# Performance work log

Measured on AMD Instinct MI355X. Metric: run time of the kernel, lower is better.

Reference implementation:

```python
import jax, jax.numpy as jnp
import numpy as np

ROPE_BASE = 10000.0

def _rope(x, positions):
    # x: (B, h, T, d); standard half-split rotary embedding with d_key = d
    d = x.shape[-1]
    inv_freq = 1.0 / (ROPE_BASE ** (jnp.arange(0, d // 2, dtype=jnp.float32) / (d // 2)))
    ang = positions.astype(jnp.float32)[:, None] * inv_freq[None, :]  # (T, d/2)
    cos, sin = jnp.cos(ang), jnp.sin(ang)
    x1, x2 = x[..., : d // 2], x[..., d // 2 :]
    return jnp.concatenate([x1 * cos - x2 * sin, x1 * sin + x2 * cos], axis=-1)


def setup_inputs() -> dict:
    key = jax.random.key(0)
    k1, k2, k3 = jax.random.split(key, 3)
    B, T, d, h = 2, 2048, 768, 8
    std = d ** -0.5
    x = jax.random.normal(k1, (B, T, d), dtype=jnp.float32)
    M = jax.random.normal(k2, (d, h * d), dtype=jnp.float32) * std
    V = jax.random.normal(k3, (d, h * d), dtype=jnp.float32) * std
    positions = jnp.arange(T, dtype=jnp.int32)
    return {"x": x, "M": M, "V": V, "positions": positions}


def reference(x, M, V, positions):
    B, T, d = x.shape
    h = M.shape[1] // d
    scale = 1.0 / jnp.sqrt(jnp.float32(d))
    # Q = RoPE(X @ M), K = RoPE(X) broadcast across heads, val = X @ V
    Q = (x @ M).reshape(B, T, h, d).transpose(0, 2, 1, 3)   # (B,h,T,d)
    val = (x @ V).reshape(B, T, h, d).transpose(0, 2, 1, 3)  # (B,h,T,d)
    K = jnp.broadcast_to(x[:, None, :, :], (B, h, T, d))     # (B,h,T,d)
    Q = _rope(Q, positions)
    K = _rope(K, positions)
    scores = jnp.einsum("bhqd,bhkd->bhqk", Q, K) * scale     # (B,h,T,T)
    causal = jnp.tril(jnp.ones((T, T), dtype=bool))          # True = keep
    scores = jnp.where(causal[None, None], scores, -jnp.inf)
    attn = jax.nn.softmax(scores, axis=-1)
    out = jnp.einsum("bhqk,bhkd->bhqd", attn, val)
    return out.sum(axis=1)  # sum over heads -> (B,T,d)
```

## Files before the change

### kernel.cpp

```cpp
#include <hip/hip_runtime.h>
#include <hip/hip_bf16.h>

typedef __bf16 bf16x8 __attribute__((ext_vector_type(8)));
typedef float f32x4 __attribute__((ext_vector_type(4)));
typedef float f32x16 __attribute__((ext_vector_type(16)));

#define SCALE 0.03608439182435161f
#define NEGINF (-1e30f)

static __device__ __forceinline__ ushort f2bf(float f) {
    union { float f; unsigned u; } v; v.f = f;
    unsigned r = (v.u + 0x7fff + ((v.u >> 16) & 1)) >> 16;
    return (ushort)r;
}
static __device__ __forceinline__ float bf2f(ushort u) {
    union { unsigned u; float f; } v; v.u = ((unsigned)u) << 16;
    return v.f;
}

static __device__ __forceinline__ void gload16(const void* g, void* lds) {
    __builtin_amdgcn_global_load_lds((const __attribute__((address_space(1))) void*)g,
                                     (__attribute__((address_space(3))) void*)lds, 16, 0, 0);
}

#define PHASEB do { asm volatile("s_waitcnt vmcnt(0) lgkmcnt(0)" ::: "memory"); \
                    __builtin_amdgcn_s_barrier(); \
                    asm volatile("" ::: "memory"); } while (0)
#define BARL do { asm volatile("s_waitcnt lgkmcnt(0)" ::: "memory"); \
                  __builtin_amdgcn_s_barrier(); \
                  asm volatile("" ::: "memory"); } while (0)

__global__ void k_convx(const float* __restrict__ x, ushort* __restrict__ xb, int n4) {
    int i = blockIdx.x * blockDim.x + threadIdx.x;
    if (i >= n4) return;
    float4 v = ((const float4*)x)[i];
    ushort4 o; o.x = f2bf(v.x); o.y = f2bf(v.y); o.z = f2bf(v.z); o.w = f2bf(v.w);
    ((ushort4*)xb)[i] = o;
}

__global__ void k_tconv(const float* __restrict__ in, ushort* __restrict__ out, int R, int C) {
    __shared__ float ts[32][33];
    int r0 = blockIdx.x * 32, c0 = blockIdx.y * 32;
    int lr = threadIdx.x >> 5, lc = threadIdx.x & 31;
#pragma unroll
    for (int i = 0; i < 4; i++) ts[lr + i * 8][lc] = in[(r0 + lr + i * 8) * C + c0 + lc];
    __syncthreads();
#pragma unroll
    for (int i = 0; i < 4; i++) out[(c0 + lr + i * 8) * R + r0 + lc] = f2bf(ts[lc][lr + i * 8]);
}

template <int EPI>
__global__ __launch_bounds__(256) void k_gemm(const ushort* __restrict__ A,
                                              const ushort* __restrict__ Bt,
                                              ushort* __restrict__ out) {
    __shared__ ushort As[128 * 32];
    __shared__ ushort Bs[128 * 32];
    const int m0 = blockIdx.x * 128, n0 = blockIdx.y * 128;
    const int tid = threadIdx.x, lane = tid & 63, wid = tid >> 6;
    const int wm = (wid >> 1) * 64, wn = (wid & 1) * 64;
    const int l15 = lane & 15, l4 = lane >> 4;
    const int srow = tid >> 2, scol = (tid & 3) * 8;
    f32x4 acc[4][4] = {};

    for (int kt = 0; kt < 768; kt += 32) {
        gload16(&A[(size_t)(m0 + srow) * 768 + kt + scol],       (char*)As + wid * 1024);
        gload16(&A[(size_t)(m0 + 64 + srow) * 768 + kt + scol],  (char*)As + 4096 + wid * 1024);
        gload16(&Bt[(size_t)(n0 + srow) * 768 + kt + scol],      (char*)Bs + wid * 1024);
        gload16(&Bt[(size_t)(n0 + 64 + srow) * 768 + kt + scol], (char*)Bs + 4096 + wid * 1024);
        PHASEB;
        bf16x8 af[4], bfr[4];
#pragma unroll
        for (int m = 0; m < 4; m++)
            af[m] = *(const bf16x8*)&As[(wm + m * 16 + l15) * 32 + l4 * 8];
#pragma unroll
        for (int n = 0; n < 4; n++)
            bfr[n] = *(const bf16x8*)&Bs[(wn + n * 16 + l15) * 32 + l4 * 8];
#pragma unroll
        for (int m = 0; m < 4; m++)
#pragma unroll
            for (int n = 0; n < 4; n++)
                acc[m][n] = __builtin_amdgcn_mfma_f32_16x16x32_bf16(af[m], bfr[n], acc[m][n], 0, 0, 0);
        BARL;
    }

#pragma unroll
    for (int m = 0; m < 4; m++) {
#pragma unroll
        for (int n = 0; n < 4; n++) {
#pragma unroll
            for (int r = 0; r < 4; r++) {
                int row = m0 + wm + m * 16 + (lane >> 4) * 4 + r;
                int col = n0 + wn + n * 16 + (lane & 15);
                float v = acc[m][n][r];
                int idx;
                if (EPI == 0) {
                    int b = row >> 11, t = row & 2047;
                    int hh = col / 768, dd = col - hh * 768;
                    idx = ((b * 8 + hh) * 2048 + t) * 768 + dd;
                } else {
                    int hh = row / 768, dd = row - hh * 768;
                    int b = col >> 11, t = col & 2047;
                    idx = ((b * 8 + hh) * 768 + dd) * 2048 + t;
                }
                out[idx] = f2bf(v);
            }
        }
    }
}

__global__ void k_ropek(const float* __restrict__ x, ushort* __restrict__ Kr,
                        const int* __restrict__ pos, float2* __restrict__ tab, int nrows) {
    int i = blockIdx.x * blockDim.x + threadIdx.x;
    int row = i / 96, j4 = (i % 96) * 4;
    if (row >= nrows) return;
    float p = (float)pos[row & 2047];
    float4 x1 = *(const float4*)&x[row * 768 + j4];
    float4 x2 = *(const float4*)&x[row * 768 + 384 + j4];
    ushort4 o1, o2;
    float a1[4] = {x1.x, x1.y, x1.z, x1.w};
    float a2[4] = {x2.x, x2.y, x2.z, x2.w};
#pragma unroll
    for (int k = 0; k < 4; k++) {
        float inv = exp2f(-(float)(j4 + k) * (13.287712379549449f / 384.0f));
        float ang = p * inv;
        float s, c; sincosf(ang, &s, &c);
        ((ushort*)&o1)[k] = f2bf(a1[k] * c - a2[k] * s);
        ((ushort*)&o2)[k] = f2bf(a1[k] * s + a2[k] * c);
        if (row < 2048) tab[(size_t)row * 384 + j4 + k] = make_float2(c * SCALE, s * SCALE);
    }
    *(ushort4*)&Kr[row * 768 + j4] = o1;
    *(ushort4*)&Kr[row * 768 + 384 + j4] = o2;
}

__global__ __launch_bounds__(512, 2) void k_attn(const ushort* Qr, const ushort* __restrict__ Kr,
                                                 const ushort* __restrict__ valT,
                                                 const float2* __restrict__ tab, ushort* Oh) {
    __shared__ alignas(128) char Qs[98304];
    __shared__ alignas(128) char pool[65536];

    const int p = blockIdx.x, hh = blockIdx.y, b = blockIdx.z;
    const int bh = b * 8 + hh;
    const int tid = threadIdx.x, lane = tid & 63, wid = tid >> 6;
    const int g = wid & 3, qh = wid >> 2;
    const int l31 = lane & 31, hi = lane >> 5;
    const int hi16 = hi << 4;

    const int row0 = tid >> 4, col16 = tid & 15;
    const int swz = (col16 << 4) ^ ((row0 & 15) << 4);

    const int arow = g * 32 + l31;
    const int qrow = qh * 32 + l31;
    const int asw = (arow & 15) << 4;
    const int qsw = (qrow & 15) << 4;

    char* Pb = pool + 32768;
    float* pmax_s = (float*)(pool + 49152);
    float* psum_s = (float*)(pool + 50176);

    const char* Kb0 = (const char*)Kr + ((size_t)(b * 2048 + row0)) * 1536 + swz;
    const char* Vb0 = (const char*)valT + ((size_t)(bh * 768 + row0)) * 4096 + swz;

    for (int ti = 0; ti < 2; ti++) {
        const int qt = ti ? (31 - p) : p;
        const int q0 = qt * 64;
        const int nkb = (qt + 2) >> 1;
        const int qg = q0 + qrow;

        const char* qsrc = (const char*)Qr + ((size_t)(bh * 2048 + q0 + row0)) * 1536 + swz;
#pragma unroll
        for (int r = 0; r < 12; r++)
            gload16(qsrc + (r >> 1) * 256 + (size_t)(r & 1) * 49152,
                    Qs + (r >> 1) * 16384 + (r & 1) * 8192 + wid * 1024);
#pragma unroll
        for (int r = 0; r < 4; r++)
            gload16(Kb0 + (size_t)r * 49152, pool + r * 8192 + wid * 1024);

        PHASEB;

        {
            const int rr = tid >> 3;
            const int gb0 = (tid & 7) * 16;
            const int rsw = (rr & 15) << 4;
            const float2* trow = tab + (size_t)(q0 + rr) * 384 + (gb0 >> 1);
#pragma unroll
            for (int c = 0; c < 3; c++) {
#pragma unroll
                for (int h2 = 0; h2 < 2; h2++) {
                    int gb = gb0 + h2 * 128;
                    char* p1 = Qs + c * 16384 + rr * 256 + (gb ^ rsw);
                    char* p2 = Qs + (c + 3) * 16384 + rr * 256 + (gb ^ rsw);
                    uint4 u1 = *(uint4*)p1, u2 = *(uint4*)p2;
                    const float4* tp = (const float4*)(trow + c * 128 + h2 * 64);
                    float4 T0 = tp[0], T1 = tp[1], T2 = tp[2], T3 = tp[3];
                    const float tf[16] = {T0.x, T0.y, T0.z, T0.w, T1.x, T1.y, T1.z, T1.w,
                                          T2.x, T2.y, T2.z, T2.w, T3.x, T3.y, T3.z, T3.w};
                    uint4 o1, o2;
                    ushort* a1 = (ushort*)&u1; ushort* a2 = (ushort*)&u2;
                    ushort* b1 = (ushort*)&o1; ushort* b2 = (ushort*)&o2;
#pragma unroll
                    for (int k = 0; k < 8; k++) {
                        float cs = tf[2 * k], sn = tf[2 * k + 1];
                        float x1 = bf2f(a1[k]), x2 = bf2f(a2[k]);
                        b1[k] = f2bf(x1 * cs - x2 * sn);
                        b2[k] = f2bf(x1 * sn + x2 * cs);
                    }
                    *(uint4*)p1 = o1; *(uint4*)p2 = o2;
                }
            }
        }
        BARL;

        float m_r = NEGINF, l_r = 0.f;
        f32x16 oacc[6] = {};

        for (int kb = 0; kb < nkb; kb++) {
            const char* kc = Kb0 + (size_t)kb * 196608;
            const char* vc = Vb0 + (size_t)kb * 256;
            const bool nx = (kb + 1 < nkb);
            const bool nm = (kb * 128 + 127 > q0);

            f32x16 sacc = {};
#pragma unroll
            for (int c = 0; c < 6; c++) {
                PHASEB;
                if (c < 5) {
#pragma unroll
                    for (int r = 0; r < 4; r++)
                        gload16(kc + (c + 1) * 256 + (size_t)r * 49152,
                                pool + ((c + 1) & 1) * 32768 + r * 8192 + wid * 1024);
                } else {
#pragma unroll
                    for (int r = 0; r < 4; r++)
                        gload16(vc + (size_t)r * 131072, pool + r * 8192 + wid * 1024);
                }
                const char* kbuf = pool + (c & 1) * 32768;
                const char* qcb = Qs + c * 16384;
                __builtin_amdgcn_s_setprio(1);
#pragma unroll
                for (int s = 0; s < 8; s++) {
                    bf16x8 a = *(const bf16x8*)(kbuf + arow * 256 + ((s * 32 + hi16) ^ asw));
                    bf16x8 bq = *(const bf16x8*)(qcb + qrow * 256 + ((s * 32 + hi16) ^ qsw));
                    sacc = __builtin_amdgcn_mfma_f32_32x32x16_bf16(a, bq, sacc, 0, 0, 0);
                }
                __builtin_amdgcn_s_setprio(0);
            }

            BARL;

            const int kbase_ = kb * 128 + g * 32 + 4 * hi;
            float mloc = NEGINF;
            if (nm) {
#pragma unroll
                for (int r = 0; r < 16; r++) {
                    int kg = kbase_ + (r & 3) + 8 * (r >> 2);
                    if (kg <= qg) mloc = fmaxf(mloc, sacc[r]);
                }
            } else {
#pragma unroll
                for (int r = 0; r < 16; r++) mloc = fmaxf(mloc, sacc[r]);
            }
            mloc = fmaxf(mloc, __shfl_xor(mloc, 32));
            if (hi == 0) pmax_s[qrow * 4 + g] = mloc;
            BARL;

            float4 pm = *(const float4*)&pmax_s[qrow * 4];
            float m_new = fmaxf(fmaxf(fmaxf(pm.x, pm.y), fmaxf(pm.z, pm.w)), m_r);
            float rv = __expf(m_r - m_new);
            float ps = 0.f; uint w[8];
            if (nm) {
#pragma unroll
                for (int j = 0; j < 8; j++) {
                    int kg0 = kbase_ + ((2 * j) & 3) + 8 * ((2 * j) >> 2);
                    int kg1 = kbase_ + ((2 * j + 1) & 3) + 8 * ((2 * j + 1) >> 2);
                    float e0 = (kg0 > qg) ? 0.f : __expf(sacc[2 * j] - m_new);
                    float e1 = (kg1 > qg) ? 0.f : __expf(sacc[2 * j + 1] - m_new);
                    ps += e0 + e1;
                    w[j] = (uint)f2bf(e0) | ((uint)f2bf(e1) << 16);
                }
            } else {
#pragma unroll
                for (int j = 0; j < 8; j++) {
                    float e0 = __expf(sacc[2 * j] - m_new);
                    float e1 = __expf(sacc[2 * j + 1] - m_new);
                    ps += e0 + e1;
                    w[j] = (uint)f2bf(e0) | ((uint)f2bf(e1) << 16);
                }
            }
            ps += __shfl_xor(ps, 32);
            if (hi == 0) psum_s[qrow * 4 + g] = ps;
#pragma unroll
            for (int j = 0; j < 4; j++) {
                uint2 pw; pw.x = w[2 * j]; pw.y = w[2 * j + 1];
                *(uint2*)(Pb + qrow * 256 + ((g * 64 + j * 16 + hi * 8) ^ qsw)) = pw;
            }
            BARL;

            float4 ps4 = *(const float4*)&psum_s[qrow * 4];
            l_r = l_r * rv + (ps4.x + ps4.y + ps4.z + ps4.w);
            m_r = m_new;
            float rs[16];
#pragma unroll
            for (int r = 0; r < 16; r++)
                rs[r] = __shfl(rv, (r & 3) + 8 * (r >> 2) + 4 * hi);
#pragma unroll
            for (int c = 0; c < 6; c++)
#pragma unroll
                for (int r = 0; r < 16; r++) oacc[c][r] *= rs[r];
            bf16x8 pa[8];
#pragma unroll
            for (int s = 0; s < 8; s++)
                pa[s] = *(const bf16x8*)(Pb + qrow * 256 + ((s * 32 + hi16) ^ qsw));

#pragma unroll
            for (int c = 0; c < 6; c++) {
                PHASEB;
                if (c < 5) {
#pragma unroll
                    for (int r = 0; r < 4; r++)
                        gload16(vc + (size_t)(c + 1) * 524288 + (size_t)r * 131072,
                                pool + ((c + 1) & 1) * 32768 + r * 8192 + wid * 1024);
                } else if (nx) {
#pragma unroll
                    for (int r = 0; r < 4; r++)
                        gload16(kc + 196608 + (size_t)r * 49152, pool + r * 8192 + wid * 1024);
                }
                const char* vbuf = pool + (c & 1) * 32768;
                __builtin_amdgcn_s_setprio(1);
#pragma unroll
                for (int s = 0; s < 8; s++) {
                    bf16x8 bv = *(const bf16x8*)(vbuf + arow * 256 + ((s * 32 + hi16) ^ asw));
                    oacc[c] = __builtin_amdgcn_mfma_f32_32x32x16_bf16(pa[s], bv, oacc[c], 0, 0, 0);
                }
                __builtin_amdgcn_s_setprio(0);
            }
        }

        float inv16[16];
#pragma unroll
        for (int r = 0; r < 16; r++)
            inv16[r] = 1.0f / __shfl(l_r, (r & 3) + 8 * (r >> 2) + 4 * hi);
        ushort* obase = Oh + ((size_t)(bh * 2048 + q0 + qh * 32)) * 768;
#pragma unroll
        for (int c = 0; c < 6; c++) {
            int dd = c * 128 + g * 32 + l31;
#pragma unroll
            for (int r = 0; r < 16; r++) {
                int rq = (r & 3) + 8 * (r >> 2) + 4 * hi;
                obase[(size_t)rq * 768 + dd] = f2bf(oacc[c][r] * inv16[r]);
            }
        }
    }
}

__global__ void k_reduce(const ushort* __restrict__ Oh, float* __restrict__ out) {
    int i = blockIdx.x * blockDim.x + threadIdx.x;
    if (i >= 786432) return;
    size_t base = (size_t)i * 4;
    int b = (base >= 1572864) ? 1 : 0;
    size_t rem = base - (size_t)b * 1572864;
    const ushort* src = Oh + (size_t)b * 8 * 1572864 + rem;
    float4 acc = {0.f, 0.f, 0.f, 0.f};
#pragma unroll
    for (int h = 0; h < 8; h++) {
        ushort4 v = *(const ushort4*)(src + (size_t)h * 1572864);
        acc.x += bf2f(v.x); acc.y += bf2f(v.y); acc.z += bf2f(v.z); acc.w += bf2f(v.w);
    }
    *(float4*)&out[base] = acc;
}

extern "C" void kernel_launch(void* const* d_in, const int* in_sizes, int n_in,
                              void* d_out, int out_size, void* d_ws, size_t ws_size,
                              hipStream_t stream) {
    const float* x = (const float*)d_in[0];
    const float* M = (const float*)d_in[1];
    const float* V = (const float*)d_in[2];
    const int* pos = (const int*)d_in[3];
    float* out = (float*)d_out;
    char* ws = (char*)d_ws;

    ushort* xb   = (ushort*)(ws);
    ushort* Mt   = (ushort*)(ws + 6291456);
    ushort* Vt   = (ushort*)(ws + 15728640);
    ushort* Qr   = (ushort*)(ws + 25165824);
    ushort* valT = (ushort*)(ws + 75497472);
    ushort* Kr   = (ushort*)(ws + 125829120);
    float2* tab  = (float2*)(ws);

    k_convx<<<3072, 256, 0, stream>>>(x, xb, 786432);
    k_tconv<<<dim3(24, 192), 256, 0, stream>>>(M, Mt, 768, 6144);
    k_tconv<<<dim3(24, 192), 256, 0, stream>>>(V, Vt, 768, 6144);
    k_gemm<0><<<dim3(32, 48), 256, 0, stream>>>(xb, Mt, Qr);
    k_gemm<1><<<dim3(48, 32), 256, 0, stream>>>(Vt, xb, valT);
    k_ropek<<<1536, 256, 0, stream>>>(x, Kr, pos, tab, 4096);
    k_attn<<<dim3(16, 8, 2), 512, 0, stream>>>(Qr, Kr, valT, tab, Qr );
    k_reduce<<<3072, 256, 0, stream>>>(Qr, out);
}
```

Baseline: 345.9 us.

## Double-buffer GEMM LDS tiles and swizzle workgroup tile mapping

The projection GEMM now keeps two LDS buffers for the A and B tiles. The global-to-LDS loads for the next k-step are issued right after the barrier, so they overlap with the MFMA work on the current tile, and the trailing barrier is dropped. Workgroup IDs are also remapped with a stride-8 swizzle to change which output tiles run at the same time, aiming for better L2 reuse. In exchange the kernel uses twice the LDS, which can lower occupancy, and the swizzle is only a valid permutation when the workgroup count is a multiple of 8.

```diff
diff --git a/kernel.cpp b/kernel.cpp
--- a/kernel.cpp
+++ b/kernel.cpp
@@ -53,35 +53,52 @@
 __global__ __launch_bounds__(256) void k_gemm(const ushort* __restrict__ A,
                                               const ushort* __restrict__ Bt,
                                               ushort* __restrict__ out) {
-    __shared__ ushort As[128 * 32];
-    __shared__ ushort Bs[128 * 32];
-    const int m0 = blockIdx.x * 128, n0 = blockIdx.y * 128;
+    __shared__ ushort As[2][128 * 32];
+    __shared__ ushort Bs[2][128 * 32];
+    const int mt = gridDim.x;
+    const int nwg = gridDim.x * gridDim.y;
+    const int wg = blockIdx.y * gridDim.x + blockIdx.x;
+    const int sw = (wg & 7) * (nwg >> 3) + (wg >> 3);
+    const int m0 = (sw % mt) * 128, n0 = (sw / mt) * 128;
+
     const int tid = threadIdx.x, lane = tid & 63, wid = tid >> 6;
     const int wm = (wid >> 1) * 64, wn = (wid & 1) * 64;
     const int l15 = lane & 15, l4 = lane >> 4;
     const int srow = tid >> 2, scol = (tid & 3) * 8;
     f32x4 acc[4][4] = {};
 
+    const ushort* Arow0 = &A[(size_t)(m0 + srow) * 768 + scol];
+    const ushort* Arow1 = &A[(size_t)(m0 + 64 + srow) * 768 + scol];
+    const ushort* Brow0 = &Bt[(size_t)(n0 + srow) * 768 + scol];
+    const ushort* Brow1 = &Bt[(size_t)(n0 + 64 + srow) * 768 + scol];
+
+#define GSTAGE(buf, kt) do { \
+        gload16(Arow0 + (kt), (char*)As[buf] + wid * 1024); \
+        gload16(Arow1 + (kt), (char*)As[buf] + 4096 + wid * 1024); \
+        gload16(Brow0 + (kt), (char*)Bs[buf] + wid * 1024); \
+        gload16(Brow1 + (kt), (char*)Bs[buf] + 4096 + wid * 1024); \
+    } while (0)
+
+    GSTAGE(0, 0);
+    int cur = 0;
     for (int kt = 0; kt < 768; kt += 32) {
-        gload16(&A[(size_t)(m0 + srow) * 768 + kt + scol],       (char*)As + wid * 1024);
-        gload16(&A[(size_t)(m0 + 64 + srow) * 768 + kt + scol],  (char*)As + 4096 + wid * 1024);
-        gload16(&Bt[(size_t)(n0 + srow) * 768 + kt + scol],      (char*)Bs + wid * 1024);
-        gload16(&Bt[(size_t)(n0 + 64 + srow) * 768 + kt + scol], (char*)Bs + 4096 + wid * 1024);
         PHASEB;
+        if (kt + 32 < 768) GSTAGE(cur ^ 1, kt + 32);
         bf16x8 af[4], bfr[4];
 #pragma unroll
         for (int m = 0; m < 4; m++)
-            af[m] = *(const bf16x8*)&As[(wm + m * 16 + l15) * 32 + l4 * 8];
+            af[m] = *(const bf16x8*)&As[cur][(wm + m * 16 + l15) * 32 + l4 * 8];
 #pragma unroll
         for (int n = 0; n < 4; n++)
-            bfr[n] = *(const bf16x8*)&Bs[(wn + n * 16 + l15) * 32 + l4 * 8];
+            bfr[n] = *(const bf16x8*)&Bs[cur][(wn + n * 16 + l15) * 32 + l4 * 8];
 #pragma unroll
         for (int m = 0; m < 4; m++)
 #pragma unroll
             for (int n = 0; n < 4; n++)
                 acc[m][n] = __builtin_amdgcn_mfma_f32_16x16x32_bf16(af[m], bfr[n], acc[m][n], 0, 0, 0);
-        BARL;
+        cur ^= 1;
     }
+#undef GSTAGE
 
 #pragma unroll
     for (int m = 0; m < 4; m++) {
```

Result: no change. 350.1 us (+1.2%).
